# Kernel optimization log

Measured on AMD Instinct MI355X. Metric: run time of the kernel, lower is better.

## Reference

```python
import jax, jax.numpy as jnp
import numpy as np

D_MODEL = 128
D_STATE = 64
L = 1024
BATCH = 32
DT_MIN, DT_MAX = 1e-3, 1e-1

# poly6 Chebyshev coeffs for GELU on domain [-5, 15]
POLY6_GELU = [6.04831644882, 8.094460228971, 1.371512430522, -0.740775295685,
              0.134773988002, 0.126019270103, -0.239569101196]
GELU_LO, GELU_HI = -5.0, 15.0


def cheb_eval(x, coeffs, lo, hi):
    t = (2.0 * x - (hi + lo)) / (hi - lo)
    t0 = jnp.ones_like(t)
    res = coeffs[0] * t0
    t1 = t
    res = res + coeffs[1] * t1
    for i in range(2, len(coeffs)):
        ti = 2.0 * t * t1 - t0
        res = res + coeffs[i] * ti
        t0, t1 = t1, ti
    return res


def setup_inputs() -> dict:
    key = jax.random.key(0)
    ks = jax.random.split(key, 8)
    u = jax.random.normal(ks[0], (BATCH, D_MODEL, L), dtype=jnp.float32)
    # S4DKernel params
    log_dt = jax.random.uniform(ks[1], (D_MODEL,), dtype=jnp.float32) * (np.log(DT_MAX) - np.log(DT_MIN)) + np.log(DT_MIN)
    log_A_real = jnp.log(0.5 * jnp.ones((D_MODEL, D_STATE), dtype=jnp.float32))
    A_imag = jnp.pi * jnp.tile(jnp.arange(D_STATE, dtype=jnp.float32), (D_MODEL, 1))
    B_re = jnp.ones((D_MODEL, D_STATE), dtype=jnp.float32)
    B_im = jnp.zeros((D_MODEL, D_STATE), dtype=jnp.float32)
    C_re = jax.random.normal(ks[2], (D_MODEL, D_STATE), dtype=jnp.float32)
    C_im = jax.random.normal(ks[3], (D_MODEL, D_STATE), dtype=jnp.float32)
    # block params
    D = jax.random.normal(ks[4], (D_MODEL,), dtype=jnp.float32)
    W1 = jax.random.normal(ks[5], (2 * D_MODEL, D_MODEL), dtype=jnp.float32) * (1.0 / np.sqrt(D_MODEL))
    b1 = jnp.zeros((2 * D_MODEL,), dtype=jnp.float32)
    Wdec = jax.random.normal(ks[6], (1, D_MODEL), dtype=jnp.float32) * (1.0 / np.sqrt(D_MODEL))
    bdec = jnp.zeros((1,), dtype=jnp.float32)
    return {"u": u, "log_dt": log_dt, "log_A_real": log_A_real, "A_imag": A_imag,
            "B_re": B_re, "B_im": B_im, "C_re": C_re, "C_im": C_im,
            "D": D, "W1": W1, "b1": b1, "Wdec": Wdec, "bdec": bdec}


def s4d_kernel(log_dt, log_A_real, A_imag, B_re, B_im, C_re, C_im, length):
    dt = jnp.exp(log_dt)                                  # (d,)
    A = -jnp.exp(log_A_real) + 1j * A_imag                # (d, n) complex
    A_bar = jnp.exp(A * dt[:, None])                      # (d, n)
    Bc = B_re + 1j * B_im
    Cc = C_re + 1j * C_im
    B_bar = (A_bar - 1.0) / A * Bc                        # (d, n)
    t = jnp.arange(length, dtype=jnp.float32)
    # A_bar ** t for integer t == exp(A * dt * t)  (branch cut cancels at integers)
    A_bar_pow = jnp.exp((A * dt[:, None])[:, :, None] * t)  # (d, n, L)
    K = jnp.sum(Cc[:, :, None] * A_bar_pow * B_bar[:, :, None], axis=1)  # (d, L)
    return jnp.real(K).astype(jnp.float32)


def reference(u, log_dt, log_A_real, A_imag, B_re, B_im, C_re, C_im, D, W1, b1, Wdec, bdec):
    d_model = u.shape[1]
    length = u.shape[2]
    K = s4d_kernel(log_dt, log_A_real, A_imag, B_re, B_im, C_re, C_im, length)  # (d, L)
    # torch F.conv1d(padding=L-1, groups=d)[..., :L] == left-padded depthwise cross-correlation
    conv = jax.lax.conv_general_dilated(
        u, K[:, None, :], window_strides=(1,), padding=[(length - 1, 0)],
        dimension_numbers=("NCH", "OIH", "NCH"), feature_group_count=d_model)  # (B, d, L)
    skip = conv + u * D[:, None]
    post_gelu = cheb_eval(skip, POLY6_GELU, GELU_LO, GELU_HI)
    # 1x1 conv to 2*d channels
    pre_gate = jnp.einsum("od,bdl->bol", W1, post_gelu) + b1[None, :, None]  # (B, 2d, L)
    a, b = jnp.split(pre_gate, 2, axis=1)
    gate = jnp.clip(0.25 * b + 0.5, 0.0, 1.0)  # linear_gate GLU
    gated = a * gate                            # (B, d, L)
    pooled = gated.mean(axis=-1)                # (B, d)
    return pooled @ Wdec.T + bdec               # (B, 1)
```

## Files before the change

kernel.cpp:

```cpp
#include <hip/hip_runtime.h>
#include <hip/hip_bf16.h>
#include <math.h>

#define D_MODEL 128
#define D_STATE 64
#define LEN 1024
#define BATCH 32

typedef short short8 __attribute__((ext_vector_type(8)));
typedef float f32x4 __attribute__((ext_vector_type(4)));

union PackU { uint4 u; short8 s; };

__device__ __forceinline__ float gelu_cheb(float x) {
    float t = (2.0f * x - 10.0f) * 0.05f;
    float r = 6.04831644882f + 8.094460228971f * t;
    float tm1 = 1.0f, tc = t;
    float t2 = 2.0f * t * tc - tm1; r += 1.371512430522f  * t2;
    float t3 = 2.0f * t * t2 - tc;  r += -0.740775295685f * t3;
    float t4 = 2.0f * t * t3 - t2;  r += 0.134773988002f  * t4;
    float t5 = 2.0f * t * t4 - t3;  r += 0.126019270103f  * t5;
    float t6 = 2.0f * t * t5 - t4;  r += -0.239569101196f * t6;
    return r;
}

__device__ __forceinline__ unsigned f2bf(float f) {
    unsigned u = __float_as_uint(f);
    return (u + 0x7FFFu + ((u >> 16) & 1u)) >> 16;
}

__global__ __launch_bounds__(256) void k_genK2(const float* __restrict__ log_dt,
                                               const float* __restrict__ log_A_real,
                                               const float* __restrict__ A_imag,
                                               const float* __restrict__ B_re,
                                               const float* __restrict__ B_im,
                                               const float* __restrict__ C_re,
                                               const float* __restrict__ C_im,
                                               const float* __restrict__ W1,
                                               short* __restrict__ w1bf,
                                               float* __restrict__ K) {
    int bid = blockIdx.x;
    int d = bid >> 3, oct = bid & 7;
    int t = threadIdx.x;

    if (t < 32) { int i = bid * 32 + t; w1bf[i] = (short)f2bf(W1[i]); }

    int w = t >> 6, lane = t & 63;
    int idx = d * D_STATE + lane;
    float dt  = expf(log_dt[d]);
    float Are = -expf(log_A_real[idx]);
    float Aim = A_imag[idx];
    float dre = Are * dt, dim = Aim * dt;
    float e = expf(dre);
    float sn, cs; sincosf(dim, &sn, &cs);
    float zre = e * cs, zim = e * sn;
    float numr = zre - 1.0f, numi = zim;
    float inv = 1.0f / (Are * Are + Aim * Aim);
    float qr = (numr * Are + numi * Aim) * inv;
    float qi = (numi * Are - numr * Aim) * inv;
    float Br = B_re[idx], Bi = B_im[idx];
    float Bbr = qr * Br - qi * Bi;
    float Bbi = qr * Bi + qi * Br;
    float Cr = C_re[idx], Ci = C_im[idx];
    float ar = Cr * Bbr - Ci * Bbi;
    float ai = Cr * Bbi + Ci * Bbr;

    int c = oct * 4 + w;
    int l0 = 32 * c;
    float fl0 = (float)l0;
    float pre = 0.f, pim = 0.f;
    if (dre * fl0 > -20.f) {
        float e0 = expf(dre * fl0);
        float s0, c0; sincosf(dim * fl0, &s0, &c0);
        pre = e0 * (ar * c0 - ai * s0);
        pim = e0 * (ar * s0 + ai * c0);
    }

    float kept = 0.f;
#pragma unroll
    for (int r = 0; r < 32; ++r) {
        float s = pre;
#pragma unroll
        for (int mm = 1; mm < 64; mm <<= 1) s += __shfl_xor(s, mm, 64);
        if (lane == r) kept = s;
        float nre = pre * zre - pim * zim;
        pim = pre * zim + pim * zre;
        pre = nre;
    }
    if (lane < 32) K[(size_t)d * LEN + l0 + lane] = kept;
}

#define US_STRIDE 1032
__global__ __launch_bounds__(256) void k_conv2(const float* __restrict__ u,
                                               const float* __restrict__ K,
                                               const float* __restrict__ Dp,
                                               short* __restrict__ pgT) {
    __shared__ unsigned P[2][1027];
    __shared__ __align__(16) short Us[16][US_STRIDE];
    int bid = blockIdx.x;
    int d  = bid >> 3;
    int nh = (bid >> 2) & 1;
    int sq = bid & 3;
    int t = threadIdx.x;

    for (int y = 512 + t; y < 1027; y += 256) { P[0][y] = 0u; P[1][y] = 0u; }

    {
        const float* kp = K + (size_t)d * LEN;
        float4 kv = ((const float4*)kp)[t];
        unsigned e0 = f2bf(kv.x), e1 = f2bf(kv.y), e2 = f2bf(kv.z), e3 = f2bf(kv.w);
        unsigned e4 = (t < 255) ? f2bf(kp[4 * t + 4]) : 0u;
        P[0][2 * t]     = e0 | (e1 << 16);
        P[0][2 * t + 1] = e2 | (e3 << 16);
        P[1][2 * t]     = e1 | (e2 << 16);
        P[1][2 * t + 1] = e3 | (e4 << 16);
    }

    {
        int r = t >> 4, c0 = (t & 15) * 64;
        const float* up = u + ((size_t)(nh * 16 + r) * D_MODEL + d) * LEN;
#pragma unroll
        for (int i = 0; i < 8; ++i) {
            float4 va = *(const float4*)&up[c0 + 8 * i];
            float4 vb = *(const float4*)&up[c0 + 8 * i + 4];
            short8 wv;
            wv[0] = (short)f2bf(va.x); wv[1] = (short)f2bf(va.y);
            wv[2] = (short)f2bf(va.z); wv[3] = (short)f2bf(va.w);
            wv[4] = (short)f2bf(vb.x); wv[5] = (short)f2bf(vb.y);
            wv[6] = (short)f2bf(vb.z); wv[7] = (short)f2bf(vb.w);
            *(short8*)&Us[r][c0 + 8 * i] = wv;
        }
    }
    __syncthreads();

    int wvu = __builtin_amdgcn_readfirstlane(t >> 6);
    int lane = t & 63;
    int m16 = lane & 15, q = lane >> 4;
    const unsigned* Pc = (m16 & 1) ? &P[0][0] : &P[1][0];

    unsigned y0[4];
    f32x4 accv[4];
#pragma unroll
    for (int j = 0; j < 4; ++j) {
        int I = sq + 4 * (wvu + 4 * j);
        int S0 = 1023 + 8 * q - 16 * I - m16;
        y0[j] = ((unsigned)S0) >> 1;
        accv[j] = (f32x4){0.f, 0.f, 0.f, 0.f};
    }

#pragma unroll
    for (int ks = 0; ks < 32; ++ks) {
        short8 bfrag = *(const short8*)&Us[m16][32 * ks + 8 * q];
#pragma unroll
        for (int j = 0; j < 4; ++j) {
            int I = sq + 4 * (wvu + 4 * j);
            if (2 * ks <= I) {
                unsigned y = y0[j] + 16 * ks;
                PackU pu;
                pu.u.x = Pc[y]; pu.u.y = Pc[y + 1]; pu.u.z = Pc[y + 2]; pu.u.w = Pc[y + 3];
                accv[j] = __builtin_amdgcn_mfma_f32_16x16x32_bf16(pu.s, bfrag, accv[j], 0, 0, 0);
            }
        }
    }

    float Dd = Dp[d];
    int b = nh * 16 + m16;
    const float* ug = u + ((size_t)b * D_MODEL + d) * LEN;
#pragma unroll
    for (int j = 0; j < 4; ++j) {
        int I = sq + 4 * (wvu + 4 * j);
        int l0 = 16 * I + 4 * q;
        float4 u4 = *(const float4*)&ug[l0];
        float v0 = gelu_cheb(accv[j][0] + u4.x * Dd);
        float v1 = gelu_cheb(accv[j][1] + u4.y * Dd);
        float v2 = gelu_cheb(accv[j][2] + u4.z * Dd);
        float v3 = gelu_cheb(accv[j][3] + u4.w * Dd);
        size_t base = ((size_t)b * LEN + l0) * D_MODEL + d;
        pgT[base + 0 * D_MODEL] = (short)f2bf(v0);
        pgT[base + 1 * D_MODEL] = (short)f2bf(v1);
        pgT[base + 2 * D_MODEL] = (short)f2bf(v2);
        pgT[base + 3 * D_MODEL] = (short)f2bf(v3);
    }
}

__global__ __launch_bounds__(256) void k_glu_mfma(const short* __restrict__ pgT,
                                                  const short* __restrict__ w1bf,
                                                  const float* __restrict__ b1,
                                                  const float* __restrict__ Wdec,
                                                  float* __restrict__ acc2) {
    __shared__ float red[4];
    int b = blockIdx.y;
    int lc = blockIdx.x;
    int l0 = lc * 64;
    int t = threadIdx.x;
    int wv = t >> 6, lane = t & 63;
    int m = lane & 15, q = lane >> 4;

    const short* wA0 = w1bf + ((2 * wv + 0) * 16 + m) * D_MODEL;
    const short* wA1 = w1bf + ((2 * wv + 1) * 16 + m) * D_MODEL;

    short8 aA0[4], aA1[4], aB0[4], aB1[4];
#pragma unroll
    for (int kki = 0; kki < 4; ++kki) {
        int ko = kki * 32 + q * 8;
        aA0[kki] = *(const short8*)(wA0 + ko);
        aA1[kki] = *(const short8*)(wA1 + ko);
        aB0[kki] = *(const short8*)(wA0 + 128 * D_MODEL + ko);
        aB1[kki] = *(const short8*)(wA1 + 128 * D_MODEL + ko);
    }

    const short* pgb = pgT + ((size_t)b * LEN + l0) * D_MODEL;

    f32x4 accA[2][4], accB[2][4];
#pragma unroll
    for (int p = 0; p < 2; ++p)
#pragma unroll
        for (int nt = 0; nt < 4; ++nt) {
            accA[p][nt] = (f32x4){0.f, 0.f, 0.f, 0.f};
            accB[p][nt] = (f32x4){0.f, 0.f, 0.f, 0.f};
        }

#pragma unroll
    for (int kki = 0; kki < 4; ++kki) {
        int ko = kki * 32 + q * 8;
        short8 bfr[4];
#pragma unroll
        for (int nt = 0; nt < 4; ++nt)
            bfr[nt] = *(const short8*)&pgb[(size_t)(nt * 16 + m) * D_MODEL + ko];
#pragma unroll
        for (int nt = 0; nt < 4; ++nt) {
            accA[0][nt] = __builtin_amdgcn_mfma_f32_16x16x32_bf16(aA0[kki], bfr[nt], accA[0][nt], 0, 0, 0);
            accA[1][nt] = __builtin_amdgcn_mfma_f32_16x16x32_bf16(aA1[kki], bfr[nt], accA[1][nt], 0, 0, 0);
            accB[0][nt] = __builtin_amdgcn_mfma_f32_16x16x32_bf16(aB0[kki], bfr[nt], accB[0][nt], 0, 0, 0);
            accB[1][nt] = __builtin_amdgcn_mfma_f32_16x16x32_bf16(aB1[kki], bfr[nt], accB[1][nt], 0, 0, 0);
        }
    }

    float s = 0.f;
#pragma unroll
    for (int p = 0; p < 2; ++p) {
        int oA = (2 * wv + p) * 16 + q * 4;
#pragma unroll
        for (int r = 0; r < 4; ++r) {
            int o = oA + r;
            float wd  = Wdec[o];
            float ba  = b1[o];
            float bb1 = b1[o + 128];
#pragma unroll
            for (int nt = 0; nt < 4; ++nt) {
                float aa  = accA[p][nt][r] + ba;
                float bbv = accB[p][nt][r] + bb1;
                float g = fminf(fmaxf(0.25f * bbv + 0.5f, 0.f), 1.f);
                s += wd * aa * g;
            }
        }
    }
#pragma unroll
    for (int off = 32; off > 0; off >>= 1) s += __shfl_down(s, off, 64);
    if (lane == 0) red[wv] = s;
    __syncthreads();
    if (t == 0) acc2[b * 16 + lc] = red[0] + red[1] + red[2] + red[3];
}

__global__ void k_finish(const float* __restrict__ acc2, const float* __restrict__ bdec,
                         float* __restrict__ out) {
    int b = threadIdx.x;
    if (b < BATCH) {
        float s = 0.f;
#pragma unroll
        for (int c = 0; c < 16; ++c) s += acc2[b * 16 + c];
        out[b] = s * (1.0f / (float)LEN) + bdec[0];
    }
}

extern "C" void kernel_launch(void* const* d_in, const int* in_sizes, int n_in,
                              void* d_out, int out_size, void* d_ws, size_t ws_size,
                              hipStream_t stream) {
    const float* u          = (const float*)d_in[0];
    const float* log_dt     = (const float*)d_in[1];
    const float* log_A_real = (const float*)d_in[2];
    const float* A_imag     = (const float*)d_in[3];
    const float* B_re       = (const float*)d_in[4];
    const float* B_im       = (const float*)d_in[5];
    const float* C_re       = (const float*)d_in[6];
    const float* C_im       = (const float*)d_in[7];
    const float* Dp         = (const float*)d_in[8];
    const float* W1         = (const float*)d_in[9];
    const float* b1         = (const float*)d_in[10];
    const float* Wdec       = (const float*)d_in[11];
    const float* bdec       = (const float*)d_in[12];
    float* out = (float*)d_out;

    float* w = (float*)d_ws;
    float* K      = w;
    float* acc2   = K + (size_t)D_MODEL * LEN;
    short* pgT    = (short*)(acc2 + 512);
    short* w1bf   = pgT + (size_t)BATCH * LEN * D_MODEL;

    k_genK2<<<D_MODEL * 8, 256, 0, stream>>>(log_dt, log_A_real, A_imag, B_re, B_im,
                                             C_re, C_im, W1, w1bf, K);
    k_conv2<<<D_MODEL * 8, 256, 0, stream>>>(u, K, Dp, pgT);
    k_glu_mfma<<<dim3(16, BATCH), 256, 0, stream>>>(pgT, w1bf, b1, Wdec, acc2);
    k_finish<<<1, 64, 0, stream>>>(acc2, bdec, out);
}
```

Measured before the change: 141.4 us.

## Pre-convert u to bf16 once and use shifted Toeplitz K copies in conv

The u-to-bf16 conversion moves into the K-generation kernel, so each conv block reads bf16 u directly from global memory instead of converting a fp32 slice into LDS. The conv kernel now keeps 8 shifted bf16 copies of K in LDS, which turns each A-fragment load into a single aligned 16-byte read in place of four scalar loads, and it trims the loop to the causally needed k-steps. K generation swaps its 32 shuffle-reduction rounds for an LDS transpose plus a per-row sum. The trade-offs are an extra bf16 u buffer written to and read from global memory, B fragments fetched from global rather than LDS, and the skip term now using the bf16-rounded u instead of fp32.

```diff
diff --git a/kernel.cpp b/kernel.cpp
--- a/kernel.cpp
+++ b/kernel.cpp
@@ -6,11 +6,11 @@
 #define D_STATE 64
 #define LEN 1024
 #define BATCH 32
+#define KC_STRIDE 1056
 
 typedef short short8 __attribute__((ext_vector_type(8)));
+typedef short short4v __attribute__((ext_vector_type(4)));
 typedef float f32x4 __attribute__((ext_vector_type(4)));
-
-union PackU { uint4 u; short8 s; };
 
 __device__ __forceinline__ float gelu_cheb(float x) {
     float t = (2.0f * x - 10.0f) * 0.05f;
@@ -29,7 +29,11 @@
     return (u + 0x7FFFu + ((u >> 16) & 1u)) >> 16;
 }
 
-__global__ __launch_bounds__(256) void k_genK2(const float* __restrict__ log_dt,
+__device__ __forceinline__ float bf2f(short s) {
+    return __uint_as_float(((unsigned)(unsigned short)s) << 16);
+}
+
+__global__ __launch_bounds__(256) void k_genK3(const float* __restrict__ log_dt,
                                                const float* __restrict__ log_A_real,
                                                const float* __restrict__ A_imag,
                                                const float* __restrict__ B_re,
@@ -37,13 +41,33 @@
                                                const float* __restrict__ C_re,
                                                const float* __restrict__ C_im,
                                                const float* __restrict__ W1,
+                                               const float* __restrict__ u,
                                                short* __restrict__ w1bf,
+                                               short* __restrict__ u_bf,
                                                float* __restrict__ K) {
+    __shared__ float Ls[128][68];
     int bid = blockIdx.x;
     int d = bid >> 3, oct = bid & 7;
     int t = threadIdx.x;
 
     if (t < 32) { int i = bid * 32 + t; w1bf[i] = (short)f2bf(W1[i]); }
+
+    {
+        size_t tid = (size_t)bid * 256 + t;
+        const float4* src = (const float4*)(u + tid * 16);
+        float4 a = src[0], b4 = src[1], c4 = src[2], d4 = src[3];
+        uint4 o0, o1;
+        o0.x = f2bf(a.x)  | (f2bf(a.y)  << 16);
+        o0.y = f2bf(a.z)  | (f2bf(a.w)  << 16);
+        o0.z = f2bf(b4.x) | (f2bf(b4.y) << 16);
+        o0.w = f2bf(b4.z) | (f2bf(b4.w) << 16);
+        o1.x = f2bf(c4.x) | (f2bf(c4.y) << 16);
+        o1.y = f2bf(c4.z) | (f2bf(c4.w) << 16);
+        o1.z = f2bf(d4.x) | (f2bf(d4.y) << 16);
+        o1.w = f2bf(d4.z) | (f2bf(d4.w) << 16);
+        uint4* dst = (uint4*)u_bf + tid * 2;
+        dst[0] = o0; dst[1] = o1;
+    }
 
     int w = t >> 6, lane = t & 63;
     int idx = d * D_STATE + lane;
@@ -65,70 +89,62 @@
     float ar = Cr * Bbr - Ci * Bbi;
     float ai = Cr * Bbi + Ci * Bbr;
 
-    int c = oct * 4 + w;
-    int l0 = 32 * c;
-    float fl0 = (float)l0;
+    int L0 = oct * 128 + w * 32;
+    float fl0 = (float)L0;
     float pre = 0.f, pim = 0.f;
-    if (dre * fl0 > -20.f) {
+    if (dre * fl0 > -30.f) {
         float e0 = expf(dre * fl0);
         float s0, c0; sincosf(dim * fl0, &s0, &c0);
         pre = e0 * (ar * c0 - ai * s0);
         pim = e0 * (ar * s0 + ai * c0);
     }
 
-    float kept = 0.f;
+    int row0 = w * 32;
 #pragma unroll
     for (int r = 0; r < 32; ++r) {
-        float s = pre;
-#pragma unroll
-        for (int mm = 1; mm < 64; mm <<= 1) s += __shfl_xor(s, mm, 64);
-        if (lane == r) kept = s;
+        Ls[row0 + r][lane] = pre;
         float nre = pre * zre - pim * zim;
         pim = pre * zim + pim * zre;
         pre = nre;
     }
-    if (lane < 32) K[(size_t)d * LEN + l0 + lane] = kept;
-}
-
-#define US_STRIDE 1032
-__global__ __launch_bounds__(256) void k_conv2(const float* __restrict__ u,
-                                               const float* __restrict__ K,
+    __syncthreads();
+
+    if (t < 128) {
+        f32x4 s4 = (f32x4){0.f, 0.f, 0.f, 0.f};
+#pragma unroll
+        for (int c = 0; c < 16; ++c) s4 += *(const f32x4*)&Ls[t][4 * c];
+        K[(size_t)d * LEN + oct * 128 + t] = s4.x + s4.y + s4.z + s4.w;
+    }
+}
+
+__global__ __launch_bounds__(256) void k_conv3(const float* __restrict__ K,
+                                               const short* __restrict__ u_bf,
                                                const float* __restrict__ Dp,
                                                short* __restrict__ pgT) {
-    __shared__ unsigned P[2][1027];
-    __shared__ __align__(16) short Us[16][US_STRIDE];
+    __shared__ __align__(16) short Kc[8 * KC_STRIDE];
     int bid = blockIdx.x;
     int d  = bid >> 3;
     int nh = (bid >> 2) & 1;
     int sq = bid & 3;
     int t = threadIdx.x;
 
-    for (int y = 512 + t; y < 1027; y += 256) { P[0][y] = 0u; P[1][y] = 0u; }
-
+    if (t < 160) {
+        int c = t / 20, y = t - c * 20;
+        ((unsigned*)&Kc[c * KC_STRIDE + 1016])[y] = 0u;
+    }
     {
         const float* kp = K + (size_t)d * LEN;
         float4 kv = ((const float4*)kp)[t];
-        unsigned e0 = f2bf(kv.x), e1 = f2bf(kv.y), e2 = f2bf(kv.z), e3 = f2bf(kv.w);
-        unsigned e4 = (t < 255) ? f2bf(kp[4 * t + 4]) : 0u;
-        P[0][2 * t]     = e0 | (e1 << 16);
-        P[0][2 * t + 1] = e2 | (e3 << 16);
-        P[1][2 * t]     = e1 | (e2 << 16);
-        P[1][2 * t + 1] = e3 | (e4 << 16);
-    }
-
-    {
-        int r = t >> 4, c0 = (t & 15) * 64;
-        const float* up = u + ((size_t)(nh * 16 + r) * D_MODEL + d) * LEN;
-#pragma unroll
-        for (int i = 0; i < 8; ++i) {
-            float4 va = *(const float4*)&up[c0 + 8 * i];
-            float4 vb = *(const float4*)&up[c0 + 8 * i + 4];
-            short8 wv;
-            wv[0] = (short)f2bf(va.x); wv[1] = (short)f2bf(va.y);
-            wv[2] = (short)f2bf(va.z); wv[3] = (short)f2bf(va.w);
-            wv[4] = (short)f2bf(vb.x); wv[5] = (short)f2bf(vb.y);
-            wv[6] = (short)f2bf(vb.z); wv[7] = (short)f2bf(vb.w);
-            *(short8*)&Us[r][c0 + 8 * i] = wv;
+        float vals[4] = {kv.x, kv.y, kv.z, kv.w};
+#pragma unroll
+        for (int mm = 0; mm < 4; ++mm) {
+            int ei = 4 * t + mm;
+            short bv = (short)f2bf(vals[mm]);
+#pragma unroll
+            for (int c = 0; c < 8; ++c) {
+                int x = ei - c;
+                if (x >= 0) Kc[c * KC_STRIDE + x] = bv;
+            }
         }
     }
     __syncthreads();
@@ -136,50 +152,49 @@
     int wvu = __builtin_amdgcn_readfirstlane(t >> 6);
     int lane = t & 63;
     int m16 = lane & 15, q = lane >> 4;
-    const unsigned* Pc = (m16 & 1) ? &P[0][0] : &P[1][0];
-
-    unsigned y0[4];
+    int cc = (7 - m16) & 7;
+    const short* Krow = Kc + cc * KC_STRIDE;
+    const short* ub = u_bf + (((size_t)(nh * 16 + m16) * D_MODEL + d) << 10);
+
+    int x0[4];
     f32x4 accv[4];
 #pragma unroll
     for (int j = 0; j < 4; ++j) {
         int I = sq + 4 * (wvu + 4 * j);
-        int S0 = 1023 + 8 * q - 16 * I - m16;
-        y0[j] = ((unsigned)S0) >> 1;
+        x0[j] = 1023 + 8 * q - 16 * I - m16 - cc;
         accv[j] = (f32x4){0.f, 0.f, 0.f, 0.f};
     }
 
-#pragma unroll
-    for (int ks = 0; ks < 32; ++ks) {
-        short8 bfrag = *(const short8*)&Us[m16][32 * ks + 8 * q];
+    int ks_end = (sq + 4 * wvu + 48) / 2 + 1;
+    if (ks_end > 32) ks_end = 32;
+    for (int ks = 0; ks < ks_end; ++ks) {
+        short8 bfrag = *(const short8*)&ub[32 * ks + 8 * q];
 #pragma unroll
         for (int j = 0; j < 4; ++j) {
             int I = sq + 4 * (wvu + 4 * j);
             if (2 * ks <= I) {
-                unsigned y = y0[j] + 16 * ks;
-                PackU pu;
-                pu.u.x = Pc[y]; pu.u.y = Pc[y + 1]; pu.u.z = Pc[y + 2]; pu.u.w = Pc[y + 3];
-                accv[j] = __builtin_amdgcn_mfma_f32_16x16x32_bf16(pu.s, bfrag, accv[j], 0, 0, 0);
+                short8 afrag = *(const short8*)&Krow[x0[j] + 32 * ks];
+                accv[j] = __builtin_amdgcn_mfma_f32_16x16x32_bf16(afrag, bfrag, accv[j], 0, 0, 0);
             }
         }
     }
 
     float Dd = Dp[d];
     int b = nh * 16 + m16;
-    const float* ug = u + ((size_t)b * D_MODEL + d) * LEN;
 #pragma unroll
     for (int j = 0; j < 4; ++j) {
         int I = sq + 4 * (wvu + 4 * j);
         int l0 = 16 * I + 4 * q;
-        float4 u4 = *(const float4*)&ug[l0];
-        float v0 = gelu_cheb(accv[j][0] + u4.x * Dd);
-        float v1 = gelu_cheb(accv[j][1] + u4.y * Dd);
-        float v2 = gelu_cheb(accv[j][2] + u4.z * Dd);
-        float v3 = gelu_cheb(accv[j][3] + u4.w * Dd);
-        size_t base = ((size_t)b * LEN + l0) * D_MODEL + d;
-        pgT[base + 0 * D_MODEL] = (short)f2bf(v0);
-        pgT[base + 1 * D_MODEL] = (short)f2bf(v1);
-        pgT[base + 2 * D_MODEL] = (short)f2bf(v2);
-        pgT[base + 3 * D_MODEL] = (short)f2bf(v3);
+        short4v us = *(const short4v*)&ub[l0];
+        float v0 = gelu_cheb(accv[j][0] + bf2f(us[0]) * Dd);
+        float v1 = gelu_cheb(accv[j][1] + bf2f(us[1]) * Dd);
+        float v2 = gelu_cheb(accv[j][2] + bf2f(us[2]) * Dd);
+        float v3 = gelu_cheb(accv[j][3] + bf2f(us[3]) * Dd);
+        size_t basep = ((size_t)b * LEN + l0) * D_MODEL + d;
+        pgT[basep + 0 * D_MODEL] = (short)f2bf(v0);
+        pgT[basep + 1 * D_MODEL] = (short)f2bf(v1);
+        pgT[basep + 2 * D_MODEL] = (short)f2bf(v2);
+        pgT[basep + 3 * D_MODEL] = (short)f2bf(v3);
     }
 }
 
@@ -294,12 +309,13 @@
     float* w = (float*)d_ws;
     float* K      = w;
     float* acc2   = K + (size_t)D_MODEL * LEN;
-    short* pgT    = (short*)(acc2 + 512);
+    short* u_bf   = (short*)(acc2 + 512);
+    short* pgT    = u_bf + (size_t)BATCH * D_MODEL * LEN;
     short* w1bf   = pgT + (size_t)BATCH * LEN * D_MODEL;
 
-    k_genK2<<<D_MODEL * 8, 256, 0, stream>>>(log_dt, log_A_real, A_imag, B_re, B_im,
-                                             C_re, C_im, W1, w1bf, K);
-    k_conv2<<<D_MODEL * 8, 256, 0, stream>>>(u, K, Dp, pgT);
+    k_genK3<<<D_MODEL * 8, 256, 0, stream>>>(log_dt, log_A_real, A_imag, B_re, B_im,
+                                             C_re, C_im, W1, u, w1bf, u_bf, K);
+    k_conv3<<<D_MODEL * 8, 256, 0, stream>>>(K, u_bf, Dp, pgT);
     k_glu_mfma<<<dim3(16, BATCH), 256, 0, stream>>>(pgT, w1bf, b1, Wdec, acc2);
     k_finish<<<1, 64, 0, stream>>>(acc2, bdec, out);
 }
```

Result: faster. 136.0 us (-3.8%).
